# Kernel tuning notes

Measured on AMD Instinct MI355X. Metric: run time of the kernel, lower is better.

The kernel has to match this reference:

```python
import jax, jax.numpy as jnp
import numpy as np

N, E = 50000, 400000
EMB, IN, HID, HEADS = 128, 128, 128, 3
RRELU_SLOPE = (1.0 / 8.0 + 1.0 / 3.0) / 2.0  # torch.rrelu eval-mode slope


def _gat_conv(h_in, src, dst, W, a_src, a_dst, b, concat):
    """PyG-style GATConv. h_in: [N, F_in]; src/dst: [E'] (self-loops included)."""
    n = h_in.shape[0]
    h = (h_in @ W).reshape(n, HEADS, -1)            # [N, H, C]
    e_src = jnp.sum(h * a_src, axis=-1)             # [N, H]
    e_dst = jnp.sum(h * a_dst, axis=-1)             # [N, H]
    e = jax.nn.leaky_relu(e_src[src] + e_dst[dst], 0.2)  # [E', H]
    # softmax over incoming edges of each target node
    m = jax.ops.segment_max(e, dst, num_segments=n)
    ex = jnp.exp(e - m[dst])
    denom = jax.ops.segment_sum(ex, dst, num_segments=n)
    alpha = ex / denom[dst]                          # [E', H]
    out = jax.ops.segment_sum(h[src] * alpha[:, :, None], dst, num_segments=n)  # [N,H,C]
    out = out.reshape(n, -1) if concat else out.mean(axis=1)
    return out + b


def _rrelu(x):
    return jnp.where(x >= 0, x, x * RRELU_SLOPE)


def setup_inputs() -> dict:
    key = jax.random.key(0)
    ks = jax.random.split(key, 16)
    d_in = IN + EMB

    def glorot(k, shape):
        fan = sum(shape)
        return jax.random.normal(k, shape, jnp.float32) * np.sqrt(2.0 / fan)

    return {
        "z": jax.random.normal(ks[0], (N, EMB), jnp.float32),
        "x": jax.random.normal(ks[1], (N, IN), jnp.float32),
        "ei": jax.random.randint(ks[2], (2, E), 0, N, jnp.int32),
        "W1": glorot(ks[3], (d_in, HEADS * HID)),
        "a1_src": glorot(ks[4], (HEADS, HID)),
        "a1_dst": glorot(ks[5], (HEADS, HID)),
        "b1": jnp.zeros((HID,), jnp.float32),                 # concat=False -> size C
        "W2": glorot(ks[6], (HID, HEADS * HID)),
        "a2_src": glorot(ks[7], (HEADS, HID)),
        "a2_dst": glorot(ks[8], (HEADS, HID)),
        "b2": jnp.zeros((HEADS * HID,), jnp.float32),         # concat=True -> size H*C
        "W_lin": glorot(ks[9], (HEADS * HID, 1)),
        "b_lin": jnp.zeros((1,), jnp.float32),
    }


def reference(z, x, ei, W1, a1_src, a1_dst, b1, W2, a2_src, a2_dst, b2, W_lin, b_lin):
    n = x.shape[0]
    loops = jnp.arange(n, dtype=ei.dtype)
    src = jnp.concatenate([ei[0], loops])  # PyG add_self_loops=True
    dst = jnp.concatenate([ei[1], loops])
    h = jnp.concatenate([z, x], axis=1)
    h = _rrelu(_gat_conv(h, src, dst, W1, a1_src, a1_dst, b1, concat=False))
    h = _rrelu(_gat_conv(h, src, dst, W2, a2_src, a2_dst, b2, concat=True))
    return jax.nn.sigmoid(h @ W_lin + b_lin)
```

## Files before the change

### kernel.cpp

```cpp
#include <hip/hip_runtime.h>
#include <stdint.h>

#define HEADS 3
#define HID 128
#define FDIM (HEADS * HID)

typedef __attribute__((ext_vector_type(8))) short bf16x8;
typedef __attribute__((ext_vector_type(4))) float f32x4;

__device__ __forceinline__ float lrelu(float x) { return x >= 0.f ? x : 0.2f * x; }
__device__ __forceinline__ float rrelu(float x) {
    const float SLOPE = (1.0f / 8.0f + 1.0f / 3.0f) * 0.5f;
    return x >= 0.f ? x : SLOPE * x;
}
__device__ __forceinline__ unsigned short f2bf(float f) {
    union { float f; unsigned u; } c; c.f = f;
    unsigned r = c.u + 0x7FFF + ((c.u >> 16) & 1);
    return (unsigned short)(r >> 16);
}
__device__ __forceinline__ float bflo(unsigned u) {
    union { unsigned u; float f; } c; c.u = u << 16; return c.f;
}
__device__ __forceinline__ float bfhi(unsigned u) {
    union { unsigned u; float f; } c; c.u = u & 0xffff0000u; return c.f;
}

__device__ __forceinline__ void gload_lds16(const void* g, void* l) {
    __builtin_amdgcn_global_load_lds(
        (const __attribute__((address_space(1))) void*)g,
        (__attribute__((address_space(3))) void*)l, 16, 0, 0);
}


__global__ void k_hist(const int* __restrict__ dst, int E, int* __restrict__ cnt) {
    for (int i = blockIdx.x * blockDim.x + threadIdx.x; i < E; i += gridDim.x * blockDim.x)
        atomicAdd(&cnt[dst[i]], 1);
}

#define SC_T 256
#define SC_E 8
#define SC_CHUNK (SC_T * SC_E)

__global__ __launch_bounds__(SC_T) void k_scan1(const int* __restrict__ cnt,
                                                int* __restrict__ exc,
                                                int* __restrict__ bsum, int n) {
    __shared__ int sm[SC_T];
    int b = blockIdx.x, t = threadIdx.x;
    int base = b * SC_CHUNK + t * SC_E;
    int v[SC_E];
    int s = 0;
#pragma unroll
    for (int i = 0; i < SC_E; i++) {
        int idx = base + i;
        v[i] = (idx < n) ? cnt[idx] : 0;
        s += v[i];
    }
    sm[t] = s;
    __syncthreads();
    for (int off = 1; off < SC_T; off <<= 1) {
        int x = (t >= off) ? sm[t - off] : 0;
        __syncthreads();
        sm[t] += x;
        __syncthreads();
    }
    int run = sm[t] - s;
    if (t == SC_T - 1) bsum[b] = sm[t];
#pragma unroll
    for (int i = 0; i < SC_E; i++) {
        int idx = base + i;
        if (idx < n) exc[idx] = run;
        run += v[i];
    }
}

__global__ __launch_bounds__(256) void k_scan2(const int* __restrict__ bsum,
                                               int* __restrict__ bpre, int nb) {
    __shared__ int sm[256];
    int t = threadIdx.x;
    int v = (t < nb) ? bsum[t] : 0;
    sm[t] = v;
    __syncthreads();
    for (int off = 1; off < 256; off <<= 1) {
        int x = (t >= off) ? sm[t - off] : 0;
        __syncthreads();
        sm[t] += x;
        __syncthreads();
    }
    if (t < nb) bpre[t + 1] = sm[t];
    if (t == 0) bpre[0] = 0;
}

__global__ void k_scan3(int* __restrict__ offs, const int* __restrict__ bpre,
                        int* __restrict__ cursor, int n, int nb) {
    int i = blockIdx.x * blockDim.x + threadIdx.x;
    if (i < n) {
        int o = offs[i] + bpre[i / SC_CHUNK];
        offs[i] = o;
        cursor[i] = o;
    }
    if (i == 0) offs[n] = bpre[nb];
}

__global__ void k_scatter(const int* __restrict__ src, const int* __restrict__ dst, int E,
                          int* __restrict__ cursor, int* __restrict__ ssrc,
                          int* __restrict__ sdst) {
    for (int i = blockIdx.x * blockDim.x + threadIdx.x; i < E; i += gridDim.x * blockDim.x) {
        int d = dst[i];
        int p = atomicAdd(&cursor[d], 1);
        ssrc[p] = src[i];
        sdst[p] = d;
    }
}


__global__ void k_cvt_wt(const float* __restrict__ W, unsigned short* __restrict__ WT,
                         int K, int Ncols) {
    int n = blockIdx.x;
    for (int k = threadIdx.x; k < K; k += blockDim.x)
        WT[(size_t)n * K + k] = f2bf(W[(size_t)k * Ncols + n]);
}


template <bool F32A>
__global__ __launch_bounds__(256) void k_gemm(
    const void* __restrict__ Ap0, const void* __restrict__ Ap1, int Nn,
    const unsigned short* __restrict__ BT,
    unsigned short* __restrict__ C,
    int K, int Ncols,
    const float* __restrict__ asrc, const float* __restrict__ adst,
    float* __restrict__ es, float* __restrict__ ed, int Nnodes) {
    __shared__ __align__(16) unsigned short As[128 * 32];
    __shared__ __align__(16) unsigned short Bs[128 * 32];
    __shared__ float esP[128][2], edP[128][2];
    int tid = threadIdx.x;
    int w = tid >> 6, lane = tid & 63;
    int row0 = blockIdx.x * 128;
    int col0 = blockIdx.y * 128;
    int wr = w >> 1, wc = w & 1;

    f32x4 acc[4][4] = {};
    int frow = lane & 15;
    int fk = (lane >> 4) * 8;

    for (int k0 = 0; k0 < K; k0 += 32) {
        if (F32A) {
            const float* zf = (const float*)Ap0;
            const float* xf = (const float*)Ap1;
            float4 va[4];
#pragma unroll
            for (int i = 0; i < 4; i++) {
                int idx = i * 256 + tid;
                int row = idx >> 3;
                int c4 = (idx & 7) * 4;
                int gr = row0 + row;
                const float* sp = (k0 < 128)
                                      ? (zf + (size_t)gr * 128 + k0 + c4)
                                      : (xf + (size_t)gr * 128 + (k0 - 128) + c4);
                va[i] = (gr < Nn) ? *(const float4*)sp
                                  : make_float4(0.f, 0.f, 0.f, 0.f);
            }
#pragma unroll
            for (int i = 0; i < 2; i++) {
                int c = (i * 4 + w) * 64 + lane;
                gload_lds16(BT + (size_t)(col0 + (c >> 2)) * K + k0 + (c & 3) * 8,
                            (char*)Bs + (i * 4 + w) * 1024);
            }
#pragma unroll
            for (int i = 0; i < 4; i++) {
                int idx = i * 256 + tid;
                unsigned short o[4] = {f2bf(va[i].x), f2bf(va[i].y),
                                       f2bf(va[i].z), f2bf(va[i].w)};
                *(uint2*)((char*)As + (size_t)idx * 8) = *(uint2*)o;
            }
        } else {
            const unsigned short* A = (const unsigned short*)Ap0;
#pragma unroll
            for (int i = 0; i < 2; i++) {
                int c = (i * 4 + w) * 64 + lane;
                gload_lds16(A + (size_t)(row0 + (c >> 2)) * K + k0 + (c & 3) * 8,
                            (char*)As + (i * 4 + w) * 1024);
            }
#pragma unroll
            for (int i = 0; i < 2; i++) {
                int c = (i * 4 + w) * 64 + lane;
                gload_lds16(BT + (size_t)(col0 + (c >> 2)) * K + k0 + (c & 3) * 8,
                            (char*)Bs + (i * 4 + w) * 1024);
            }
        }
        asm volatile("s_waitcnt vmcnt(0)" ::: "memory");
        __syncthreads();

        bf16x8 af[4], bfr[4];
#pragma unroll
        for (int m = 0; m < 4; m++)
            af[m] = *(const bf16x8*)&As[(wr * 64 + m * 16 + frow) * 32 + fk];
#pragma unroll
        for (int n = 0; n < 4; n++)
            bfr[n] = *(const bf16x8*)&Bs[(wc * 64 + n * 16 + frow) * 32 + fk];
#pragma unroll
        for (int m = 0; m < 4; m++)
#pragma unroll
            for (int n = 0; n < 4; n++)
                acc[m][n] = __builtin_amdgcn_mfma_f32_16x16x32_bf16(af[m], bfr[n], acc[m][n], 0, 0, 0);
        __syncthreads();
    }

    int ccol = lane & 15, crow = (lane >> 4) * 4;

#pragma unroll
    for (int m = 0; m < 4; m++)
#pragma unroll
        for (int n = 0; n < 4; n++)
#pragma unroll
            for (int j = 0; j < 4; j++) {
                int r = row0 + wr * 64 + m * 16 + crow + j;
                int cc = col0 + wc * 64 + n * 16 + ccol;
                C[(size_t)r * Ncols + cc] = f2bf(acc[m][n][j]);
            }

    int head = blockIdx.y;
    float as4[4], ad4[4];
#pragma unroll
    for (int n = 0; n < 4; n++) {
        int col_sub = wc * 64 + n * 16 + ccol;
        as4[n] = asrc[head * HID + col_sub];
        ad4[n] = adst[head * HID + col_sub];
    }
#pragma unroll
    for (int m = 0; m < 4; m++)
#pragma unroll
        for (int j = 0; j < 4; j++) {
            float ps = 0.f, pd = 0.f;
#pragma unroll
            for (int n = 0; n < 4; n++) {
                float v = acc[m][n][j];
                ps = fmaf(v, as4[n], ps);
                pd = fmaf(v, ad4[n], pd);
            }
#pragma unroll
            for (int off = 1; off < 16; off <<= 1) {
                ps += __shfl_xor(ps, off);
                pd += __shfl_xor(pd, off);
            }
            if (ccol == 0) {
                int row_sub = wr * 64 + m * 16 + crow + j;
                esP[row_sub][wc] = ps;
                edP[row_sub][wc] = pd;
            }
        }
    __syncthreads();
    if (tid < 128) {
        int r = row0 + tid;
        if (r < Nnodes) {
            es[(size_t)r * 3 + head] = esP[tid][0] + esP[tid][1];
            ed[(size_t)r * 3 + head] = edP[tid][0] + edP[tid][1];
        }
    }
}


__global__ void k_edge_w(const int* __restrict__ ssrc, const int* __restrict__ sdst,
                         const float* __restrict__ es, const float* __restrict__ ed,
                         float4* __restrict__ w4, int E) {
    for (int j = blockIdx.x * blockDim.x + threadIdx.x; j < E; j += gridDim.x * blockDim.x) {
        int s = ssrc[j], d = sdst[j];
        float w0 = __expf(lrelu(es[s * 3 + 0] + ed[d * 3 + 0]));
        float w1 = __expf(lrelu(es[s * 3 + 1] + ed[d * 3 + 1]));
        float w2 = __expf(lrelu(es[s * 3 + 2] + ed[d * 3 + 2]));
        w4[j] = make_float4(w0, w1, w2, 0.f);
    }
}


#define EDGE_UNROLL4(body)                                                       \
    int j = j0;                                                                  \
    for (; j + 4 <= j1; j += 4) {                                                \
        int si[4]; float4 wv[4]; unsigned uu[4][3];                              \
        _Pragma("unroll") for (int e = 0; e < 4; e++) si[e] = ssrc[j + e];       \
        _Pragma("unroll") for (int e = 0; e < 4; e++) wv[e] = w4[j + e];         \
        _Pragma("unroll") for (int e = 0; e < 4; e++) {                          \
            const unsigned* rp = Hu + (size_t)si[e] * 192 + L;                   \
            uu[e][0] = rp[0]; uu[e][1] = rp[64]; uu[e][2] = rp[128];             \
        }                                                                        \
        _Pragma("unroll") for (int e = 0; e < 4; e++) { body(wv[e], uu[e]) }     \
    }                                                                            \
    for (; j < j1; j++) {                                                        \
        int s1_ = ssrc[j]; float4 w_ = w4[j];                                    \
        const unsigned* rp = Hu + (size_t)s1_ * 192 + L;                         \
        unsigned u_[3] = {rp[0], rp[64], rp[128]};                               \
        { body(w_, u_) }                                                         \
    }

#define ACC3(wv, uv)                                                             \
    a0[0] = fmaf(wv.x, bflo(uv[0]), a0[0]); a1[0] = fmaf(wv.x, bfhi(uv[0]), a1[0]); \
    a0[1] = fmaf(wv.y, bflo(uv[1]), a0[1]); a1[1] = fmaf(wv.y, bfhi(uv[1]), a1[1]); \
    a0[2] = fmaf(wv.z, bflo(uv[2]), a0[2]); a1[2] = fmaf(wv.z, bfhi(uv[2]), a1[2]); \
    den0 += wv.x; den1 += wv.y; den2 += wv.z;

__global__ __launch_bounds__(256) void k_agg_mean(const unsigned* __restrict__ Hu,
                                                  const float4* __restrict__ w4,
                                                  const float* __restrict__ es,
                                                  const float* __restrict__ ed,
                                                  const int* __restrict__ offs,
                                                  const int* __restrict__ ssrc,
                                                  const float* __restrict__ b,
                                                  unsigned* __restrict__ out, int Nn) {
    int L = threadIdx.x & 63;
    int wstep = gridDim.x * 4;
    for (int n = blockIdx.x * 4 + (threadIdx.x >> 6); n < Nn; n += wstep) {
        float s0 = __expf(lrelu(es[n * 3 + 0] + ed[n * 3 + 0]));
        float s1 = __expf(lrelu(es[n * 3 + 1] + ed[n * 3 + 1]));
        float s2 = __expf(lrelu(es[n * 3 + 2] + ed[n * 3 + 2]));
        float den0 = s0, den1 = s1, den2 = s2;
        const unsigned* rp = Hu + (size_t)n * 192 + L;
        unsigned u0 = rp[0], u1 = rp[64], u2 = rp[128];
        float a0[3] = {s0 * bflo(u0), s1 * bflo(u1), s2 * bflo(u2)};
        float a1[3] = {s0 * bfhi(u0), s1 * bfhi(u1), s2 * bfhi(u2)};
        int j0 = offs[n], j1 = offs[n + 1];
        EDGE_UNROLL4(ACC3)
        float iv0 = 1.f / den0, iv1 = 1.f / den1, iv2 = 1.f / den2;
        int c0 = 2 * L;
        float2 bb = *(const float2*)&b[c0];
        float m0 = (a0[0] * iv0 + a0[1] * iv1 + a0[2] * iv2) * (1.f / 3.f) + bb.x;
        float m1 = (a1[0] * iv0 + a1[1] * iv1 + a1[2] * iv2) * (1.f / 3.f) + bb.y;
        unsigned short o[2] = {f2bf(rrelu(m0)), f2bf(rrelu(m1))};
        out[(size_t)n * 64 + L] = *(unsigned*)o;
    }
}

__global__ __launch_bounds__(256) void k_agg_cat_final(const unsigned* __restrict__ Hu,
                                                       const float4* __restrict__ w4,
                                                       const float* __restrict__ es,
                                                       const float* __restrict__ ed,
                                                       const int* __restrict__ offs,
                                                       const int* __restrict__ ssrc,
                                                       const float* __restrict__ b,
                                                       const float* __restrict__ Wl,
                                                       const float* __restrict__ bl,
                                                       float* __restrict__ out, int Nn) {
    int L = threadIdx.x & 63;
    int wstep = gridDim.x * 4;
    for (int n = blockIdx.x * 4 + (threadIdx.x >> 6); n < Nn; n += wstep) {
        float s0 = __expf(lrelu(es[n * 3 + 0] + ed[n * 3 + 0]));
        float s1 = __expf(lrelu(es[n * 3 + 1] + ed[n * 3 + 1]));
        float s2 = __expf(lrelu(es[n * 3 + 2] + ed[n * 3 + 2]));
        float den0 = s0, den1 = s1, den2 = s2;
        const unsigned* rp = Hu + (size_t)n * 192 + L;
        unsigned u0 = rp[0], u1 = rp[64], u2 = rp[128];
        float a0[3] = {s0 * bflo(u0), s1 * bflo(u1), s2 * bflo(u2)};
        float a1[3] = {s0 * bfhi(u0), s1 * bfhi(u1), s2 * bfhi(u2)};
        int j0 = offs[n], j1 = offs[n + 1];
        EDGE_UNROLL4(ACC3)
        float ivv[3] = {1.f / den0, 1.f / den1, 1.f / den2};
        float p = 0.f;
#pragma unroll
        for (int k = 0; k < 3; k++) {
            int col = k * HID + 2 * L;
            float2 bb = *(const float2*)&b[col];
            float2 wl = *(const float2*)&Wl[col];
            float r0 = rrelu(a0[k] * ivv[k] + bb.x);
            float r1 = rrelu(a1[k] * ivv[k] + bb.y);
            p = fmaf(r0, wl.x, p);
            p = fmaf(r1, wl.y, p);
        }
#pragma unroll
        for (int off = 32; off > 0; off >>= 1) p += __shfl_down(p, off);
        if (L == 0) out[n] = 1.f / (1.f + __expf(-(p + bl[0])));
    }
}


extern "C" void kernel_launch(void* const* d_in, const int* in_sizes, int n_in,
                              void* d_out, int out_size, void* d_ws, size_t ws_size,
                              hipStream_t stream) {
    const float* z   = (const float*)d_in[0];
    const float* x   = (const float*)d_in[1];
    const int*   ei  = (const int*)d_in[2];
    const float* W1  = (const float*)d_in[3];
    const float* a1s = (const float*)d_in[4];
    const float* a1d = (const float*)d_in[5];
    const float* b1  = (const float*)d_in[6];
    const float* W2  = (const float*)d_in[7];
    const float* a2s = (const float*)d_in[8];
    const float* a2d = (const float*)d_in[9];
    const float* b2  = (const float*)d_in[10];
    const float* Wl  = (const float*)d_in[11];
    const float* bl  = (const float*)d_in[12];
    float* outp = (float*)d_out;

    int Nn = in_sizes[0] / 128;
    int E  = in_sizes[2] / 2;
    int Mpad = (Nn + 127) & ~127;
    int nb = (Nn + SC_CHUNK - 1) / SC_CHUNK;

    char* p = (char*)d_ws;
    auto carve = [&](size_t bytes) -> char* {
        char* r = p;
        p += (bytes + 255) & ~(size_t)255;
        return r;
    };
    int*            offs   = (int*)carve((size_t)(Nn + 1) * 4);
    int*            cursor = (int*)carve((size_t)Nn * 4);
    int*            ssrc   = (int*)carve((size_t)E * 4);
    int*            sdst   = (int*)carve((size_t)E * 4);
    int*            bsum   = (int*)carve((size_t)(nb + 1) * 4);
    int*            bpre   = (int*)carve((size_t)(nb + 1) * 4);
    float*          e1s    = (float*)carve((size_t)Nn * 3 * 4);
    float*          e1d    = (float*)carve((size_t)Nn * 3 * 4);
    float4*         w4     = (float4*)carve((size_t)E * 16);
    unsigned short* W1T    = (unsigned short*)carve((size_t)FDIM * 256 * 2);
    unsigned short* W2T    = (unsigned short*)carve((size_t)FDIM * 128 * 2);
    unsigned short* Hbf    = (unsigned short*)carve((size_t)Mpad * FDIM * 2);
    unsigned short* H2in   = (unsigned short*)carve((size_t)Mpad * 128 * 2);

    const int* srcI = ei;
    const int* dstI = ei + E;

    hipMemsetAsync(cursor, 0, (size_t)Nn * 4, stream);
    k_hist<<<1024, 256, 0, stream>>>(dstI, E, cursor);
    k_scan1<<<nb, SC_T, 0, stream>>>(cursor, offs, bsum, Nn);
    k_scan2<<<1, 256, 0, stream>>>(bsum, bpre, nb);
    k_scan3<<<(Nn + 255) / 256, 256, 0, stream>>>(offs, bpre, cursor, Nn, nb);
    k_scatter<<<1024, 256, 0, stream>>>(srcI, dstI, E, cursor, ssrc, sdst);

    k_cvt_wt<<<FDIM, 256, 0, stream>>>(W1, W1T, 256, FDIM);
    k_cvt_wt<<<FDIM, 128, 0, stream>>>(W2, W2T, 128, FDIM);
    hipMemsetAsync(H2in + (size_t)Nn * 128, 0, (size_t)(Mpad - Nn) * 128 * 2, stream);

    dim3 gg(Mpad / 128, FDIM / 128);

    k_gemm<true><<<gg, 256, 0, stream>>>(z, x, Nn, W1T, Hbf, 256, FDIM,
                                         a1s, a1d, e1s, e1d, Nn);
    k_edge_w<<<1024, 256, 0, stream>>>(ssrc, sdst, e1s, e1d, w4, E);
    k_agg_mean<<<2048, 256, 0, stream>>>((const unsigned*)Hbf, w4, e1s, e1d, offs,
                                         ssrc, b1, (unsigned*)H2in, Nn);

    k_gemm<false><<<gg, 256, 0, stream>>>(H2in, nullptr, Mpad, W2T, Hbf, 128, FDIM,
                                          a2s, a2d, e1s, e1d, Nn);
    k_edge_w<<<1024, 256, 0, stream>>>(ssrc, sdst, e1s, e1d, w4, E);
    k_agg_cat_final<<<2048, 256, 0, stream>>>((const unsigned*)Hbf, w4, e1s, e1d, offs,
                                              ssrc, b2, Wl, bl, outp, Nn);
}
```

Before: 254.7 us.

## Halve GEMM row tile to 64 and prefetch fp32 A tile across k-steps

The GEMM row tile shrinks from 128 to 64 rows per block, doubling the grid to raise occupancy and CU coverage for the two projection GEMMs. In the fp32-input variant, the next k-slice of z/x is loaded into registers after the barrier so its global latency overlaps the MFMA work of the current slice. The cost is more blocks re-reading the B weight tiles, and less MFMA reuse per A/B fragment load.

Result: faster. 248.5 us (-2.5%).

```diff
diff --git a/kernel.cpp b/kernel.cpp
--- a/kernel.cpp
+++ b/kernel.cpp
@@ -129,44 +129,44 @@
     int K, int Ncols,
     const float* __restrict__ asrc, const float* __restrict__ adst,
     float* __restrict__ es, float* __restrict__ ed, int Nnodes) {
-    __shared__ __align__(16) unsigned short As[128 * 32];
+    __shared__ __align__(16) unsigned short As[64 * 32];
     __shared__ __align__(16) unsigned short Bs[128 * 32];
-    __shared__ float esP[128][2], edP[128][2];
+    __shared__ float esP[64][2], edP[64][2];
     int tid = threadIdx.x;
     int w = tid >> 6, lane = tid & 63;
-    int row0 = blockIdx.x * 128;
-    int col0 = blockIdx.y * 128;
+    int row0 = blockIdx.x * 64;
+    int head = blockIdx.y;
+    int col0 = head * 128;
     int wr = w >> 1, wc = w & 1;
 
-    f32x4 acc[4][4] = {};
+    f32x4 acc[2][4] = {};
     int frow = lane & 15;
     int fk = (lane >> 4) * 8;
 
+    const float* zf = (const float*)Ap0;
+    const float* xf = (const float*)Ap1;
+    float4 va[2];
+    if (F32A) {
+#pragma unroll
+        for (int i = 0; i < 2; i++) {
+            int idx = i * 256 + tid;
+            int row = idx >> 3, c4 = (idx & 7) * 4;
+            int gr = row0 + row;
+            const float* sp = zf + (size_t)gr * 128 + c4;
+            va[i] = (gr < Nn) ? *(const float4*)sp : make_float4(0.f, 0.f, 0.f, 0.f);
+        }
+    }
+
     for (int k0 = 0; k0 < K; k0 += 32) {
+#pragma unroll
+        for (int i = 0; i < 2; i++) {
+            int c = (i * 4 + w) * 64 + lane;
+            gload_lds16(BT + (size_t)(col0 + (c >> 2)) * K + k0 + (c & 3) * 8,
+                        (char*)Bs + (i * 4 + w) * 1024);
+        }
         if (F32A) {
-            const float* zf = (const float*)Ap0;
-            const float* xf = (const float*)Ap1;
-            float4 va[4];
-#pragma unroll
-            for (int i = 0; i < 4; i++) {
-                int idx = i * 256 + tid;
-                int row = idx >> 3;
-                int c4 = (idx & 7) * 4;
-                int gr = row0 + row;
-                const float* sp = (k0 < 128)
-                                      ? (zf + (size_t)gr * 128 + k0 + c4)
-                                      : (xf + (size_t)gr * 128 + (k0 - 128) + c4);
-                va[i] = (gr < Nn) ? *(const float4*)sp
-                                  : make_float4(0.f, 0.f, 0.f, 0.f);
-            }
 #pragma unroll
             for (int i = 0; i < 2; i++) {
-                int c = (i * 4 + w) * 64 + lane;
-                gload_lds16(BT + (size_t)(col0 + (c >> 2)) * K + k0 + (c & 3) * 8,
-                            (char*)Bs + (i * 4 + w) * 1024);
-            }
-#pragma unroll
-            for (int i = 0; i < 4; i++) {
                 int idx = i * 256 + tid;
                 unsigned short o[4] = {f2bf(va[i].x), f2bf(va[i].y),
                                        f2bf(va[i].z), f2bf(va[i].w)};
@@ -174,31 +174,36 @@
             }
         } else {
             const unsigned short* A = (const unsigned short*)Ap0;
+            int c = tid;
+            gload_lds16(A + (size_t)(row0 + (c >> 2)) * K + k0 + (c & 3) * 8,
+                        (char*)As + w * 1024);
+        }
+        asm volatile("s_waitcnt vmcnt(0)" ::: "memory");
+        __syncthreads();
+
+        if (F32A && (k0 + 32 < K)) {
+            int kn = k0 + 32;
 #pragma unroll
             for (int i = 0; i < 2; i++) {
-                int c = (i * 4 + w) * 64 + lane;
-                gload_lds16(A + (size_t)(row0 + (c >> 2)) * K + k0 + (c & 3) * 8,
-                            (char*)As + (i * 4 + w) * 1024);
-            }
-#pragma unroll
-            for (int i = 0; i < 2; i++) {
-                int c = (i * 4 + w) * 64 + lane;
-                gload_lds16(BT + (size_t)(col0 + (c >> 2)) * K + k0 + (c & 3) * 8,
-                            (char*)Bs + (i * 4 + w) * 1024);
-            }
-        }
-        asm volatile("s_waitcnt vmcnt(0)" ::: "memory");
-        __syncthreads();
-
-        bf16x8 af[4], bfr[4];
-#pragma unroll
-        for (int m = 0; m < 4; m++)
-            af[m] = *(const bf16x8*)&As[(wr * 64 + m * 16 + frow) * 32 + fk];
+                int idx = i * 256 + tid;
+                int row = idx >> 3, c4 = (idx & 7) * 4;
+                int gr = row0 + row;
+                const float* sp = (kn < 128)
+                                      ? (zf + (size_t)gr * 128 + kn + c4)
+                                      : (xf + (size_t)gr * 128 + (kn - 128) + c4);
+                va[i] = (gr < Nn) ? *(const float4*)sp : make_float4(0.f, 0.f, 0.f, 0.f);
+            }
+        }
+
+        bf16x8 af[2], bfr[4];
+#pragma unroll
+        for (int m = 0; m < 2; m++)
+            af[m] = *(const bf16x8*)&As[(wr * 32 + m * 16 + frow) * 32 + fk];
 #pragma unroll
         for (int n = 0; n < 4; n++)
             bfr[n] = *(const bf16x8*)&Bs[(wc * 64 + n * 16 + frow) * 32 + fk];
 #pragma unroll
-        for (int m = 0; m < 4; m++)
+        for (int m = 0; m < 2; m++)
 #pragma unroll
             for (int n = 0; n < 4; n++)
                 acc[m][n] = __builtin_amdgcn_mfma_f32_16x16x32_bf16(af[m], bfr[n], acc[m][n], 0, 0, 0);
@@ -208,17 +213,16 @@
     int ccol = lane & 15, crow = (lane >> 4) * 4;
 
 #pragma unroll
-    for (int m = 0; m < 4; m++)
+    for (int m = 0; m < 2; m++)
 #pragma unroll
         for (int n = 0; n < 4; n++)
 #pragma unroll
             for (int j = 0; j < 4; j++) {
-                int r = row0 + wr * 64 + m * 16 + crow + j;
+                int r = row0 + wr * 32 + m * 16 + crow + j;
                 int cc = col0 + wc * 64 + n * 16 + ccol;
                 C[(size_t)r * Ncols + cc] = f2bf(acc[m][n][j]);
             }
 
-    int head = blockIdx.y;
     float as4[4], ad4[4];
 #pragma unroll
     for (int n = 0; n < 4; n++) {
@@ -227,7 +231,7 @@
         ad4[n] = adst[head * HID + col_sub];
     }
 #pragma unroll
-    for (int m = 0; m < 4; m++)
+    for (int m = 0; m < 2; m++)
 #pragma unroll
         for (int j = 0; j < 4; j++) {
             float ps = 0.f, pd = 0.f;
@@ -243,13 +247,13 @@
                 pd += __shfl_xor(pd, off);
             }
             if (ccol == 0) {
-                int row_sub = wr * 64 + m * 16 + crow + j;
+                int row_sub = wr * 32 + m * 16 + crow + j;
                 esP[row_sub][wc] = ps;
                 edP[row_sub][wc] = pd;
             }
         }
     __syncthreads();
-    if (tid < 128) {
+    if (tid < 64) {
         int r = row0 + tid;
         if (r < Nnodes) {
             es[(size_t)r * 3 + head] = esP[tid][0] + esP[tid][1];
@@ -427,7 +431,7 @@
     k_cvt_wt<<<FDIM, 128, 0, stream>>>(W2, W2T, 128, FDIM);
     hipMemsetAsync(H2in + (size_t)Nn * 128, 0, (size_t)(Mpad - Nn) * 128 * 2, stream);
 
-    dim3 gg(Mpad / 128, FDIM / 128);
+    dim3 gg(Mpad / 64, FDIM / 128);
 
     k_gemm<true><<<gg, 256, 0, stream>>>(z, x, Nn, W1T, Hbf, 256, FDIM,
                                          a1s, a1d, e1s, e1d, Nn);
```
